# Performance work log

Measured on AMD Instinct MI355X. Metric: run time of the kernel, lower is better.

Reference implementation:

```python
import jax, jax.numpy as jnp
import numpy as np

D_MODEL = 768
NUM_HEADS = 12
D_HEAD = D_MODEL // NUM_HEADS


def setup_inputs() -> dict:
    key = jax.random.key(0)
    ks = jax.random.split(key, 12)
    B, S = 2, 2048
    s = 1.0 / np.sqrt(D_MODEL)
    inp = {
        "query": jax.random.normal(ks[0], (B, S, D_MODEL), dtype=jnp.float32),
        "key": jax.random.normal(ks[1], (B, S, D_MODEL), dtype=jnp.float32),
        "value": jax.random.normal(ks[2], (B, S, D_MODEL), dtype=jnp.float32),
        "mask": jax.random.randint(ks[3], (B, 1, 1, S), 0, 2, dtype=jnp.int32),
        "Wq": jax.random.normal(ks[4], (D_MODEL, D_MODEL), dtype=jnp.float32) * s,
        "bq": jnp.zeros((D_MODEL,), dtype=jnp.float32),
        "Wk": jax.random.normal(ks[5], (D_MODEL, D_MODEL), dtype=jnp.float32) * s,
        "bk": jnp.zeros((D_MODEL,), dtype=jnp.float32),
        "Wv": jax.random.normal(ks[6], (D_MODEL, D_MODEL), dtype=jnp.float32) * s,
        "bv": jnp.zeros((D_MODEL,), dtype=jnp.float32),
        "Wo": jax.random.normal(ks[7], (D_MODEL, D_MODEL), dtype=jnp.float32) * s,
        "bo": jnp.zeros((D_MODEL,), dtype=jnp.float32),
    }
    return inp


def _split_heads(x):
    # [B, S, D] -> [B, H, S, Dh]
    B, S, _ = x.shape
    return x.reshape(B, S, NUM_HEADS, D_HEAD).transpose(0, 2, 1, 3)


def reference(query, key, value, mask, Wq, bq, Wk, bk, Wv, bv, Wo, bo):
    q = _split_heads(query @ Wq + bq)
    k = _split_heads(key @ Wk + bk)
    v = _split_heads(value @ Wv + bv)
    scores = jnp.einsum("bhqd,bhkd->bhqk", q, k) / jnp.sqrt(jnp.float32(D_HEAD))
    scores = jnp.where(mask == 0, -jnp.inf, scores)
    attn = jax.nn.softmax(scores, axis=-1)  # dropout is identity at inference
    ctx = jnp.einsum("bhqk,bhkd->bhqd", attn, v)
    B, _, S, _ = ctx.shape
    ctx = ctx.transpose(0, 2, 1, 3).reshape(B, S, D_MODEL)
    return ctx @ Wo + bo
```

## Files before the change

kernel.cpp:

```cpp
#include <hip/hip_runtime.h>
#include <stdint.h>

#define D_MODEL 768
#define SEQ     2048
#define BATCH   2
#define NHEAD   12
#define DHEAD   64
#define MROWS   (BATCH * SEQ)

typedef __bf16 bf16x8 __attribute__((ext_vector_type(8)));
typedef float  f32x4  __attribute__((ext_vector_type(4)));
typedef unsigned short u16;
typedef u16 u16x4 __attribute__((ext_vector_type(4)));
typedef uint32_t u32;

__device__ __forceinline__ u16 f32_to_bf16(float x) {
    u32 u = __float_as_uint(x);
    u32 r = (u + 0x7FFFu + ((u >> 16) & 1u)) >> 16;
    return (u16)r;
}
__device__ __forceinline__ float bf16_to_f32(u16 h) {
    return __uint_as_float(((u32)h) << 16);
}
__device__ __forceinline__ void split2(float x, u16 &hi, u16 &lo) {
    hi = f32_to_bf16(x);
    lo = f32_to_bf16(x - bf16_to_f32(hi));
}
__device__ __forceinline__ u32 pack2(float a, float b) {
    return ((u32)f32_to_bf16(b) << 16) | (u32)f32_to_bf16(a);
}

__device__ __forceinline__ void stage16(const u16* g, const u16* l) {
    __builtin_amdgcn_global_load_lds(
        (const __attribute__((address_space(1))) u32*)g,
        (__attribute__((address_space(3))) u32*)l,
        16, 0, 0);
}

#define QSCALE 0.1803368801111204f
#define MSHIFT 20.0f

__global__ void prep_split_x(const float* __restrict__ q, const float* __restrict__ k,
                             const float* __restrict__ v, u16* __restrict__ xbase)
{
    const int t = blockIdx.y;
    const float* src = (t == 0) ? q : (t == 1) ? k : v;
    const size_t P = (size_t)MROWS * D_MODEL;
    u16* xh = xbase + (size_t)t * 2 * P;
    u16* xl = xh + P;
    size_t idx = ((size_t)blockIdx.x * 256 + threadIdx.x) * 4;
    float4 val = *reinterpret_cast<const float4*>(&src[idx]);
    float vv[4] = {val.x, val.y, val.z, val.w};
    u16x4 h4, l4;
    #pragma unroll
    for (int j = 0; j < 4; ++j) { u16 h, l; split2(vv[j], h, l); h4[j] = h; l4[j] = l; }
    *reinterpret_cast<u16x4*>(&xh[idx]) = h4;
    *reinterpret_cast<u16x4*>(&xl[idx]) = l4;
}

__global__ void prep_wt(const float* __restrict__ Wq, const float* __restrict__ Wk,
                        const float* __restrict__ Wv, const float* __restrict__ Wo,
                        u16* __restrict__ wtbase)
{
    const int w = blockIdx.z;
    const float* W = (w == 0) ? Wq : (w == 1) ? Wk : (w == 2) ? Wv : Wo;
    const size_t WP = (size_t)D_MODEL * D_MODEL;
    u16* th = wtbase + (size_t)w * 2 * WP;
    u16* tl = th + WP;

    __shared__ float tile[32][33];
    const int tx = threadIdx.x & 31, ty = threadIdx.x >> 5;
    const int n0 = blockIdx.x * 32, k0 = blockIdx.y * 32;
    #pragma unroll
    for (int r = 0; r < 4; ++r) {
        int kk = k0 + ty + r * 8;
        tile[ty + r * 8][tx] = W[(size_t)kk * D_MODEL + n0 + tx];
    }
    __syncthreads();
    #pragma unroll
    for (int r = 0; r < 4; ++r) {
        int n = n0 + ty + r * 8;
        float v = tile[tx][ty + r * 8];
        u16 h, l; split2(v, h, l);
        th[(size_t)n * D_MODEL + k0 + tx] = h;
        tl[(size_t)n * D_MODEL + k0 + tx] = l;
    }
}

__global__ void prep_bias(const int* __restrict__ Mask, float* __restrict__ BiasM)
{
    int i = blockIdx.x * 256 + threadIdx.x;
    BiasM[i] = (Mask[i] == 0) ? -3e38f : -MSHIFT;
}

__global__ __launch_bounds__(256, 4) void gemm3(
    const u16* __restrict__ Ah0, const u16* __restrict__ Al0,
    const u16* __restrict__ Ah1, const u16* __restrict__ Al1,
    const u16* __restrict__ Ah2, const u16* __restrict__ Al2,
    const u16* __restrict__ Bh0, const u16* __restrict__ Bl0,
    const u16* __restrict__ Bh1, const u16* __restrict__ Bl1,
    const u16* __restrict__ Bh2, const u16* __restrict__ Bl2,
    const float* __restrict__ bias0, const float* __restrict__ bias1,
    const float* __restrict__ bias2,
    u16* __restrict__ Qhl, u16* __restrict__ Khl, u16* __restrict__ Vt,
    float* __restrict__ Out, int mode)
{
    const int z = (mode == 3) ? 3 : (int)blockIdx.z;
    const u16 *GAh, *GAl, *GBh, *GBl; const float* Bias;
    if (z == 1)      { GAh = Ah1; GAl = Al1; GBh = Bh1; GBl = Bl1; Bias = bias1; }
    else if (z == 2) { GAh = Ah2; GAl = Al2; GBh = Bh2; GBl = Bl2; Bias = bias2; }
    else             { GAh = Ah0; GAl = Al0; GBh = Bh0; GBl = Bl0; Bias = bias0; }

    const int m0 = blockIdx.y * 128;
    const int n0 = blockIdx.x * 64;
    const int tid  = threadIdx.x;
    const int wave = tid >> 6, lane = tid & 63;
    const int quad = lane >> 4, l16 = lane & 15;
    const int wm = wave & 1, wn = wave >> 1;

    __shared__ u16 sAh[128 * 32];
    __shared__ u16 sAl[128 * 32];
    __shared__ u16 sBh[64 * 32];
    __shared__ u16 sBl[64 * 32];

    const int srow = lane >> 2;
    const int sc8  = (lane & 3) * 8;

    f32x4 acc[4][2] = {};

    for (int k0 = 0; k0 < D_MODEL; k0 += 32) {
        {
            #pragma unroll
            for (int i = 0; i < 2; ++i) {
                int row = wave * 32 + i * 16 + srow;
                size_t ga = (size_t)(m0 + row) * D_MODEL + k0 + sc8;
                int ldst = (wave * 32 + i * 16) * 32;
                stage16(&GAh[ga], &sAh[ldst]);
                stage16(&GAl[ga], &sAl[ldst]);
            }
            int row = wave * 16 + srow;
            size_t gb = (size_t)(n0 + row) * D_MODEL + k0 + sc8;
            int ldst = (wave * 16) * 32;
            stage16(&GBh[gb], &sBh[ldst]);
            stage16(&GBl[gb], &sBl[ldst]);
        }
        asm volatile("s_waitcnt vmcnt(0)" ::: "memory");
        __syncthreads();

        bf16x8 afh[4], afl[4], bfh[2], bfl[2];
        #pragma unroll
        for (int t = 0; t < 4; ++t) {
            int ar = wm * 64 + t * 16 + l16;
            afh[t] = *reinterpret_cast<const bf16x8*>(&sAh[ar * 32 + quad * 8]);
            afl[t] = *reinterpret_cast<const bf16x8*>(&sAl[ar * 32 + quad * 8]);
        }
        #pragma unroll
        for (int t = 0; t < 2; ++t) {
            int bc = wn * 32 + t * 16 + l16;
            bfh[t] = *reinterpret_cast<const bf16x8*>(&sBh[bc * 32 + quad * 8]);
            bfl[t] = *reinterpret_cast<const bf16x8*>(&sBl[bc * 32 + quad * 8]);
        }
        #pragma unroll
        for (int mt = 0; mt < 4; ++mt) {
            #pragma unroll
            for (int nt = 0; nt < 2; ++nt) {
                f32x4 a = acc[mt][nt];
                a = __builtin_amdgcn_mfma_f32_16x16x32_bf16(afh[mt], bfh[nt], a, 0, 0, 0);
                a = __builtin_amdgcn_mfma_f32_16x16x32_bf16(afh[mt], bfl[nt], a, 0, 0, 0);
                a = __builtin_amdgcn_mfma_f32_16x16x32_bf16(afl[mt], bfh[nt], a, 0, 0, 0);
                acc[mt][nt] = a;
            }
        }
        __syncthreads();
    }

    #pragma unroll
    for (int nt = 0; nt < 2; ++nt) {
        int n = n0 + wn * 32 + nt * 16 + l16;
        float bv = Bias[n];
        #pragma unroll
        for (int mt = 0; mt < 4; ++mt) {
            #pragma unroll
            for (int r = 0; r < 4; ++r) {
                int m = m0 + wm * 64 + mt * 16 + quad * 4 + r;
                float v = acc[mt][nt][r] + bv;
                if (mode == 3) {
                    Out[(size_t)m * D_MODEL + n] = v;
                } else {
                    int b = m >> 11, s = m & (SEQ - 1);
                    int h = n >> 6, d = n & 63;
                    size_t bh = (size_t)(b * NHEAD + h);
                    if (z == 0) {
                        u16 hi, lo; split2(v * QSCALE, hi, lo);
                        u16* base = &Qhl[(bh * SEQ + s) * 128];
                        base[d] = hi; base[d + 64] = lo;
                    } else if (z == 1) {
                        u16 hi, lo; split2(v, hi, lo);
                        u16* base = &Khl[(bh * SEQ + s) * 128];
                        base[d] = hi; base[d + 64] = lo;
                    } else {
                        Vt[(bh * DHEAD + d) * SEQ + s] = f32_to_bf16(v);
                    }
                }
            }
        }
    }
}

__global__ __launch_bounds__(256, 6) void attn_kernel(
    const u16* __restrict__ Qhl, const u16* __restrict__ Khl, const u16* __restrict__ Vt,
    const float* __restrict__ BiasM, float* __restrict__ Opart,
    float* __restrict__ Lpart)
{
    const int qt   = blockIdx.x;
    const int bh   = blockIdx.y;
    const int half = blockIdx.z;
    const int b    = bh / NHEAD;
    const int tid  = threadIdx.x;
    const int wave = tid >> 6, lane = tid & 63;
    const int quad = lane >> 4, l16 = lane & 15;

    __shared__ u16 sK[4 * 2048];
    __shared__ u16 sV[2 * 2048];

    const u16* qbase = &Qhl[((size_t)bh * SEQ + qt * 64 + wave * 16 + l16) * 128];
    bf16x8 qh0 = *reinterpret_cast<const bf16x8*>(&qbase[quad * 8]);
    bf16x8 qh1 = *reinterpret_cast<const bf16x8*>(&qbase[32 + quad * 8]);
    bf16x8 ql0 = *reinterpret_cast<const bf16x8*>(&qbase[64 + quad * 8]);
    bf16x8 ql1 = *reinterpret_cast<const bf16x8*>(&qbase[96 + quad * 8]);

    float lrow = 0.f;
    f32x4 oacc[4] = {};

    const float* biasb = &BiasM[b * SEQ];
    const int srcl0 = (((quad * 2) & 3) << 4) | l16;
    const int srcl1 = (((quad * 2 + 1) & 3) << 4) | l16;
    const bool selhi = (quad >> 1) != 0;

    const int strow = wave * 16 + (lane >> 2);
    const int stc8  = (lane & 3) * 8;
    const u16* kgb = &Khl[(size_t)bh * SEQ * 128];
    const u16* vgb = &Vt[(size_t)bh * DHEAD * SEQ];

    const int kvbeg = half * (SEQ / 2);
    for (int kv0 = kvbeg; kv0 < kvbeg + SEQ / 2; kv0 += 64) {
        #pragma unroll
        for (int j = 0; j < 4; ++j)
            stage16(&kgb[(size_t)(kv0 + strow) * 128 + j * 32 + stc8],
                    &sK[j * 2048 + wave * 512]);
        #pragma unroll
        for (int j = 0; j < 2; ++j)
            stage16(&vgb[(size_t)strow * SEQ + kv0 + j * 32 + stc8],
                    &sV[j * 2048 + wave * 512]);
        asm volatile("s_waitcnt vmcnt(0)" ::: "memory");
        __syncthreads();

        f32x4 sacc[4];
        #pragma unroll
        for (int mt = 0; mt < 4; ++mt) {
            float4 b4 = *reinterpret_cast<const float4*>(
                &biasb[kv0 + mt * 16 + quad * 4]);
            sacc[mt][0] = b4.x; sacc[mt][1] = b4.y;
            sacc[mt][2] = b4.z; sacc[mt][3] = b4.w;
        }
        #pragma unroll
        for (int mt = 0; mt < 4; ++mt) {
            const int rb = (mt * 16 + l16) * 32 + quad * 8;
            bf16x8 kh0 = *reinterpret_cast<const bf16x8*>(&sK[rb]);
            bf16x8 kh1 = *reinterpret_cast<const bf16x8*>(&sK[2048 + rb]);
            bf16x8 kl0 = *reinterpret_cast<const bf16x8*>(&sK[4096 + rb]);
            bf16x8 kl1 = *reinterpret_cast<const bf16x8*>(&sK[6144 + rb]);
            f32x4 s = sacc[mt];
            s = __builtin_amdgcn_mfma_f32_16x16x32_bf16(kh0, qh0, s, 0, 0, 0);
            s = __builtin_amdgcn_mfma_f32_16x16x32_bf16(kh1, qh1, s, 0, 0, 0);
            s = __builtin_amdgcn_mfma_f32_16x16x32_bf16(kh0, ql0, s, 0, 0, 0);
            s = __builtin_amdgcn_mfma_f32_16x16x32_bf16(kh1, ql1, s, 0, 0, 0);
            s = __builtin_amdgcn_mfma_f32_16x16x32_bf16(kl0, qh0, s, 0, 0, 0);
            s = __builtin_amdgcn_mfma_f32_16x16x32_bf16(kl1, qh1, s, 0, 0, 0);
            sacc[mt] = s;
        }

        u32 pLo[4], pHi[4];
        #pragma unroll
        for (int mt = 0; mt < 4; ++mt) {
            float p0 = exp2f(sacc[mt][0]);
            float p1 = exp2f(sacc[mt][1]);
            float p2 = exp2f(sacc[mt][2]);
            float p3 = exp2f(sacc[mt][3]);
            lrow += (p0 + p1) + (p2 + p3);
            pLo[mt] = pack2(p0, p1);
            pHi[mt] = pack2(p2, p3);
        }

        union FU { u32 u[4]; bf16x8 v; } fr[2];
        #pragma unroll
        for (int f = 0; f < 2; ++f) {
            u32 a, bb;
            a  = (u32)__shfl((int)pLo[2 * f],     srcl0, 64);
            bb = (u32)__shfl((int)pLo[2 * f + 1], srcl0, 64);
            fr[f].u[0] = selhi ? bb : a;
            a  = (u32)__shfl((int)pHi[2 * f],     srcl0, 64);
            bb = (u32)__shfl((int)pHi[2 * f + 1], srcl0, 64);
            fr[f].u[1] = selhi ? bb : a;
            a  = (u32)__shfl((int)pLo[2 * f],     srcl1, 64);
            bb = (u32)__shfl((int)pLo[2 * f + 1], srcl1, 64);
            fr[f].u[2] = selhi ? bb : a;
            a  = (u32)__shfl((int)pHi[2 * f],     srcl1, 64);
            bb = (u32)__shfl((int)pHi[2 * f + 1], srcl1, 64);
            fr[f].u[3] = selhi ? bb : a;
        }

        #pragma unroll
        for (int dt = 0; dt < 4; ++dt) {
            const int rb = (dt * 16 + l16) * 32 + quad * 8;
            bf16x8 vb0 = *reinterpret_cast<const bf16x8*>(&sV[rb]);
            bf16x8 vb1 = *reinterpret_cast<const bf16x8*>(&sV[2048 + rb]);
            oacc[dt] = __builtin_amdgcn_mfma_f32_16x16x32_bf16(vb0, fr[0].v, oacc[dt], 0, 0, 0);
            oacc[dt] = __builtin_amdgcn_mfma_f32_16x16x32_bf16(vb1, fr[1].v, oacc[dt], 0, 0, 0);
        }
        __syncthreads();
    }

    lrow += __shfl_xor(lrow, 16, 64);
    lrow += __shfl_xor(lrow, 32, 64);

    size_t rowb = ((size_t)(half * (BATCH * NHEAD) + bh)) * SEQ
                + qt * 64 + wave * 16 + l16;
    float* ob = &Opart[rowb * 64];
    #pragma unroll
    for (int dt = 0; dt < 4; ++dt)
        *reinterpret_cast<f32x4*>(&ob[dt * 16 + quad * 4]) = oacc[dt];
    if (quad == 0) Lpart[rowb] = lrow;
}

__global__ void attn_combine(const float* __restrict__ Opart,
                             const float* __restrict__ Lpart,
                             u16* __restrict__ CTXh, u16* __restrict__ CTXl)
{
    const int NROW = BATCH * NHEAD * SEQ;
    int t = blockIdx.x * 256 + threadIdx.x;
    int row = t >> 4;
    int d0 = (t & 15) << 2;
    float inv = 1.f / (Lpart[row] + Lpart[NROW + row]);
    f32x4 O0 = *reinterpret_cast<const f32x4*>(&Opart[(size_t)row * 64 + d0]);
    f32x4 O1 = *reinterpret_cast<const f32x4*>(&Opart[((size_t)NROW + row) * 64 + d0]);
    int bh = row >> 11, q = row & (SEQ - 1);
    int b = bh / NHEAD, h = bh % NHEAD;
    size_t off = ((size_t)(b * SEQ + q)) * D_MODEL + h * DHEAD + d0;
    u16x4 h4, l4;
    #pragma unroll
    for (int j = 0; j < 4; ++j) {
        float val = (O0[j] + O1[j]) * inv;
        u16 hi, lo; split2(val, hi, lo);
        h4[j] = hi; l4[j] = lo;
    }
    *reinterpret_cast<u16x4*>(&CTXh[off]) = h4;
    *reinterpret_cast<u16x4*>(&CTXl[off]) = l4;
}

extern "C" void kernel_launch(void* const* d_in, const int* in_sizes, int n_in,
                              void* d_out, int out_size, void* d_ws, size_t ws_size,
                              hipStream_t stream)
{
    const float* query = (const float*)d_in[0];
    const float* key   = (const float*)d_in[1];
    const float* value = (const float*)d_in[2];
    const int*   mask  = (const int*)d_in[3];
    const float* Wq = (const float*)d_in[4];
    const float* bq = (const float*)d_in[5];
    const float* Wk = (const float*)d_in[6];
    const float* bk = (const float*)d_in[7];
    const float* Wv = (const float*)d_in[8];
    const float* bv = (const float*)d_in[9];
    const float* Wo = (const float*)d_in[10];
    const float* bo = (const float*)d_in[11];

    char* ws = (char*)d_ws;
    const size_t P2  = (size_t)MROWS * D_MODEL * 2;
    const size_t WP2 = (size_t)D_MODEL * D_MODEL * 2;

    u16* Xbase = (u16*)ws;
    u16* Xh_q = Xbase;                       u16* Xl_q = (u16*)((char*)Xh_q + P2);
    u16* Xh_k = (u16*)((char*)Xbase + 2*P2); u16* Xl_k = (u16*)((char*)Xh_k + P2);
    u16* Xh_v = (u16*)((char*)Xbase + 4*P2); u16* Xl_v = (u16*)((char*)Xh_v + P2);

    char* wtb = ws + 6 * P2;
    u16* Wh_q = (u16*)wtb;                   u16* Wl_q = (u16*)(wtb + WP2);
    u16* Wh_k = (u16*)(wtb + 2*WP2);         u16* Wl_k = (u16*)(wtb + 3*WP2);
    u16* Wh_v = (u16*)(wtb + 4*WP2);         u16* Wl_v = (u16*)(wtb + 5*WP2);
    u16* Wh_o = (u16*)(wtb + 6*WP2);         u16* Wl_o = (u16*)(wtb + 7*WP2);

    char* qb = wtb + 8 * WP2;
    const size_t QK_BYTES = (size_t)BATCH * NHEAD * SEQ * 128 * 2;
    u16* QhlBuf = (u16*)qb;
    u16* KhlBuf = (u16*)(qb + QK_BYTES);
    u16* VtBuf  = (u16*)(qb + 2 * QK_BYTES);

    char* tail = qb + 2 * QK_BYTES + QK_BYTES / 2;
    float* BiasM = (float*)tail;
    float* Lpart = (float*)(tail + 16384);

    float* Opart = (float*)Xh_k;
    u16* CTXh = Xh_q; u16* CTXl = Xl_q;

    float* out = (float*)d_out;
    dim3 blk(256, 1, 1);

    prep_split_x<<<dim3(3072, 3), blk, 0, stream>>>(query, key, value, Xbase);
    prep_wt<<<dim3(24, 24, 4), blk, 0, stream>>>(Wq, Wk, Wv, Wo, (u16*)wtb);
    prep_bias<<<dim3(16), blk, 0, stream>>>(mask, BiasM);

    gemm3<<<dim3(12, 32, 3), blk, 0, stream>>>(
        Xh_q, Xl_q, Xh_k, Xl_k, Xh_v, Xl_v,
        Wh_q, Wl_q, Wh_k, Wl_k, Wh_v, Wl_v,
        bq, bk, bv, QhlBuf, KhlBuf, VtBuf, nullptr, 0);

    attn_kernel<<<dim3(32, 24, 2), blk, 0, stream>>>(
        QhlBuf, KhlBuf, VtBuf, BiasM, Opart, Lpart);

    attn_combine<<<dim3(3072), blk, 0, stream>>>(Opart, Lpart, CTXh, CTXl);

    gemm3<<<dim3(12, 32, 1), blk, 0, stream>>>(
        CTXh, CTXl, nullptr, nullptr, nullptr, nullptr,
        Wh_o, Wl_o, nullptr, nullptr, nullptr, nullptr,
        bo, nullptr, nullptr, nullptr, nullptr, nullptr, out, 3);
}
```

Baseline: 310.8 us.

## Process two query groups per wave in attention and swap GEMM grid order

The attention kernel now gives each wave 32 query rows (two 16-row groups) instead of 16, so each staged K/V tile in shared memory is reused twice. This halves the number of blocks and the global-to-LDS traffic per query. The cost is doubled accumulator registers, so occupancy is lowered to 3 blocks per CU. Separately, the GEMM grid is transposed so consecutive blocks walk along M rather than N, which changes L2 reuse of the weight tiles.

```diff
diff --git a/kernel.cpp b/kernel.cpp
--- a/kernel.cpp
+++ b/kernel.cpp
@@ -111,8 +111,8 @@
     else if (z == 2) { GAh = Ah2; GAl = Al2; GBh = Bh2; GBl = Bl2; Bias = bias2; }
     else             { GAh = Ah0; GAl = Al0; GBh = Bh0; GBl = Bl0; Bias = bias0; }
 
-    const int m0 = blockIdx.y * 128;
-    const int n0 = blockIdx.x * 64;
+    const int m0 = blockIdx.x * 128;
+    const int n0 = blockIdx.y * 64;
     const int tid  = threadIdx.x;
     const int wave = tid >> 6, lane = tid & 63;
     const int quad = lane >> 4, l16 = lane & 15;
@@ -207,7 +207,7 @@
     }
 }
 
-__global__ __launch_bounds__(256, 6) void attn_kernel(
+__global__ __launch_bounds__(256, 3) void attn_kernel(
     const u16* __restrict__ Qhl, const u16* __restrict__ Khl, const u16* __restrict__ Vt,
     const float* __restrict__ BiasM, float* __restrict__ Opart,
     float* __restrict__ Lpart)
@@ -223,14 +223,18 @@
     __shared__ u16 sK[4 * 2048];
     __shared__ u16 sV[2 * 2048];
 
-    const u16* qbase = &Qhl[((size_t)bh * SEQ + qt * 64 + wave * 16 + l16) * 128];
-    bf16x8 qh0 = *reinterpret_cast<const bf16x8*>(&qbase[quad * 8]);
-    bf16x8 qh1 = *reinterpret_cast<const bf16x8*>(&qbase[32 + quad * 8]);
-    bf16x8 ql0 = *reinterpret_cast<const bf16x8*>(&qbase[64 + quad * 8]);
-    bf16x8 ql1 = *reinterpret_cast<const bf16x8*>(&qbase[96 + quad * 8]);
-
-    float lrow = 0.f;
-    f32x4 oacc[4] = {};
+    bf16x8 qh0[2], qh1[2], ql0[2], ql1[2];
+    #pragma unroll
+    for (int g = 0; g < 2; ++g) {
+        const u16* qbase = &Qhl[((size_t)bh * SEQ + qt * 128 + wave * 32 + g * 16 + l16) * 128];
+        qh0[g] = *reinterpret_cast<const bf16x8*>(&qbase[quad * 8]);
+        qh1[g] = *reinterpret_cast<const bf16x8*>(&qbase[32 + quad * 8]);
+        ql0[g] = *reinterpret_cast<const bf16x8*>(&qbase[64 + quad * 8]);
+        ql1[g] = *reinterpret_cast<const bf16x8*>(&qbase[96 + quad * 8]);
+    }
+
+    float lrow[2] = {0.f, 0.f};
+    f32x4 oacc[2][4] = {};
 
     const float* biasb = &BiasM[b * SEQ];
     const int srcl0 = (((quad * 2) & 3) << 4) | l16;
@@ -255,82 +259,90 @@
         asm volatile("s_waitcnt vmcnt(0)" ::: "memory");
         __syncthreads();
 
-        f32x4 sacc[4];
+        f32x4 binit[4];
         #pragma unroll
         for (int mt = 0; mt < 4; ++mt) {
             float4 b4 = *reinterpret_cast<const float4*>(
                 &biasb[kv0 + mt * 16 + quad * 4]);
-            sacc[mt][0] = b4.x; sacc[mt][1] = b4.y;
-            sacc[mt][2] = b4.z; sacc[mt][3] = b4.w;
-        }
-        #pragma unroll
-        for (int mt = 0; mt < 4; ++mt) {
-            const int rb = (mt * 16 + l16) * 32 + quad * 8;
-            bf16x8 kh0 = *reinterpret_cast<const bf16x8*>(&sK[rb]);
-            bf16x8 kh1 = *reinterpret_cast<const bf16x8*>(&sK[2048 + rb]);
-            bf16x8 kl0 = *reinterpret_cast<const bf16x8*>(&sK[4096 + rb]);
-            bf16x8 kl1 = *reinterpret_cast<const bf16x8*>(&sK[6144 + rb]);
-            f32x4 s = sacc[mt];
-            s = __builtin_amdgcn_mfma_f32_16x16x32_bf16(kh0, qh0, s, 0, 0, 0);
-            s = __builtin_amdgcn_mfma_f32_16x16x32_bf16(kh1, qh1, s, 0, 0, 0);
-            s = __builtin_amdgcn_mfma_f32_16x16x32_bf16(kh0, ql0, s, 0, 0, 0);
-            s = __builtin_amdgcn_mfma_f32_16x16x32_bf16(kh1, ql1, s, 0, 0, 0);
-            s = __builtin_amdgcn_mfma_f32_16x16x32_bf16(kl0, qh0, s, 0, 0, 0);
-            s = __builtin_amdgcn_mfma_f32_16x16x32_bf16(kl1, qh1, s, 0, 0, 0);
-            sacc[mt] = s;
-        }
-
-        u32 pLo[4], pHi[4];
-        #pragma unroll
-        for (int mt = 0; mt < 4; ++mt) {
-            float p0 = exp2f(sacc[mt][0]);
-            float p1 = exp2f(sacc[mt][1]);
-            float p2 = exp2f(sacc[mt][2]);
-            float p3 = exp2f(sacc[mt][3]);
-            lrow += (p0 + p1) + (p2 + p3);
-            pLo[mt] = pack2(p0, p1);
-            pHi[mt] = pack2(p2, p3);
-        }
-
-        union FU { u32 u[4]; bf16x8 v; } fr[2];
-        #pragma unroll
-        for (int f = 0; f < 2; ++f) {
-            u32 a, bb;
-            a  = (u32)__shfl((int)pLo[2 * f],     srcl0, 64);
-            bb = (u32)__shfl((int)pLo[2 * f + 1], srcl0, 64);
-            fr[f].u[0] = selhi ? bb : a;
-            a  = (u32)__shfl((int)pHi[2 * f],     srcl0, 64);
-            bb = (u32)__shfl((int)pHi[2 * f + 1], srcl0, 64);
-            fr[f].u[1] = selhi ? bb : a;
-            a  = (u32)__shfl((int)pLo[2 * f],     srcl1, 64);
-            bb = (u32)__shfl((int)pLo[2 * f + 1], srcl1, 64);
-            fr[f].u[2] = selhi ? bb : a;
-            a  = (u32)__shfl((int)pHi[2 * f],     srcl1, 64);
-            bb = (u32)__shfl((int)pHi[2 * f + 1], srcl1, 64);
-            fr[f].u[3] = selhi ? bb : a;
-        }
-
-        #pragma unroll
-        for (int dt = 0; dt < 4; ++dt) {
-            const int rb = (dt * 16 + l16) * 32 + quad * 8;
-            bf16x8 vb0 = *reinterpret_cast<const bf16x8*>(&sV[rb]);
-            bf16x8 vb1 = *reinterpret_cast<const bf16x8*>(&sV[2048 + rb]);
-            oacc[dt] = __builtin_amdgcn_mfma_f32_16x16x32_bf16(vb0, fr[0].v, oacc[dt], 0, 0, 0);
-            oacc[dt] = __builtin_amdgcn_mfma_f32_16x16x32_bf16(vb1, fr[1].v, oacc[dt], 0, 0, 0);
+            binit[mt][0] = b4.x; binit[mt][1] = b4.y;
+            binit[mt][2] = b4.z; binit[mt][3] = b4.w;
+        }
+
+        #pragma unroll
+        for (int g = 0; g < 2; ++g) {
+            f32x4 sacc[4];
+            #pragma unroll
+            for (int mt = 0; mt < 4; ++mt) {
+                const int rb = (mt * 16 + l16) * 32 + quad * 8;
+                bf16x8 kh0 = *reinterpret_cast<const bf16x8*>(&sK[rb]);
+                bf16x8 kh1 = *reinterpret_cast<const bf16x8*>(&sK[2048 + rb]);
+                bf16x8 kl0 = *reinterpret_cast<const bf16x8*>(&sK[4096 + rb]);
+                bf16x8 kl1 = *reinterpret_cast<const bf16x8*>(&sK[6144 + rb]);
+                f32x4 s = binit[mt];
+                s = __builtin_amdgcn_mfma_f32_16x16x32_bf16(kh0, qh0[g], s, 0, 0, 0);
+                s = __builtin_amdgcn_mfma_f32_16x16x32_bf16(kh1, qh1[g], s, 0, 0, 0);
+                s = __builtin_amdgcn_mfma_f32_16x16x32_bf16(kh0, ql0[g], s, 0, 0, 0);
+                s = __builtin_amdgcn_mfma_f32_16x16x32_bf16(kh1, ql1[g], s, 0, 0, 0);
+                s = __builtin_amdgcn_mfma_f32_16x16x32_bf16(kl0, qh0[g], s, 0, 0, 0);
+                s = __builtin_amdgcn_mfma_f32_16x16x32_bf16(kl1, qh1[g], s, 0, 0, 0);
+                sacc[mt] = s;
+            }
+
+            u32 pLo[4], pHi[4];
+            #pragma unroll
+            for (int mt = 0; mt < 4; ++mt) {
+                float p0 = exp2f(sacc[mt][0]);
+                float p1 = exp2f(sacc[mt][1]);
+                float p2 = exp2f(sacc[mt][2]);
+                float p3 = exp2f(sacc[mt][3]);
+                lrow[g] += (p0 + p1) + (p2 + p3);
+                pLo[mt] = pack2(p0, p1);
+                pHi[mt] = pack2(p2, p3);
+            }
+
+            union FU { u32 u[4]; bf16x8 v; } fr[2];
+            #pragma unroll
+            for (int f = 0; f < 2; ++f) {
+                u32 a, bb;
+                a  = (u32)__shfl((int)pLo[2 * f],     srcl0, 64);
+                bb = (u32)__shfl((int)pLo[2 * f + 1], srcl0, 64);
+                fr[f].u[0] = selhi ? bb : a;
+                a  = (u32)__shfl((int)pHi[2 * f],     srcl0, 64);
+                bb = (u32)__shfl((int)pHi[2 * f + 1], srcl0, 64);
+                fr[f].u[1] = selhi ? bb : a;
+                a  = (u32)__shfl((int)pLo[2 * f],     srcl1, 64);
+                bb = (u32)__shfl((int)pLo[2 * f + 1], srcl1, 64);
+                fr[f].u[2] = selhi ? bb : a;
+                a  = (u32)__shfl((int)pHi[2 * f],     srcl1, 64);
+                bb = (u32)__shfl((int)pHi[2 * f + 1], srcl1, 64);
+                fr[f].u[3] = selhi ? bb : a;
+            }
+
+            #pragma unroll
+            for (int dt = 0; dt < 4; ++dt) {
+                const int rb = (dt * 16 + l16) * 32 + quad * 8;
+                bf16x8 vb0 = *reinterpret_cast<const bf16x8*>(&sV[rb]);
+                bf16x8 vb1 = *reinterpret_cast<const bf16x8*>(&sV[2048 + rb]);
+                oacc[g][dt] = __builtin_amdgcn_mfma_f32_16x16x32_bf16(vb0, fr[0].v, oacc[g][dt], 0, 0, 0);
+                oacc[g][dt] = __builtin_amdgcn_mfma_f32_16x16x32_bf16(vb1, fr[1].v, oacc[g][dt], 0, 0, 0);
+            }
         }
         __syncthreads();
     }
 
-    lrow += __shfl_xor(lrow, 16, 64);
-    lrow += __shfl_xor(lrow, 32, 64);
-
-    size_t rowb = ((size_t)(half * (BATCH * NHEAD) + bh)) * SEQ
-                + qt * 64 + wave * 16 + l16;
-    float* ob = &Opart[rowb * 64];
-    #pragma unroll
-    for (int dt = 0; dt < 4; ++dt)
-        *reinterpret_cast<f32x4*>(&ob[dt * 16 + quad * 4]) = oacc[dt];
-    if (quad == 0) Lpart[rowb] = lrow;
+    #pragma unroll
+    for (int g = 0; g < 2; ++g) {
+        float l = lrow[g];
+        l += __shfl_xor(l, 16, 64);
+        l += __shfl_xor(l, 32, 64);
+        size_t rowb = ((size_t)(half * (BATCH * NHEAD) + bh)) * SEQ
+                    + qt * 128 + wave * 32 + g * 16 + l16;
+        float* ob = &Opart[rowb * 64];
+        #pragma unroll
+        for (int dt = 0; dt < 4; ++dt)
+            *reinterpret_cast<f32x4*>(&ob[dt * 16 + quad * 4]) = oacc[g][dt];
+        if (quad == 0) Lpart[rowb] = l;
+    }
 }
 
 __global__ void attn_combine(const float* __restrict__ Opart,
@@ -410,17 +422,17 @@
     prep_wt<<<dim3(24, 24, 4), blk, 0, stream>>>(Wq, Wk, Wv, Wo, (u16*)wtb);
     prep_bias<<<dim3(16), blk, 0, stream>>>(mask, BiasM);
 
-    gemm3<<<dim3(12, 32, 3), blk, 0, stream>>>(
+    gemm3<<<dim3(32, 12, 3), blk, 0, stream>>>(
         Xh_q, Xl_q, Xh_k, Xl_k, Xh_v, Xl_v,
         Wh_q, Wl_q, Wh_k, Wl_k, Wh_v, Wl_v,
         bq, bk, bv, QhlBuf, KhlBuf, VtBuf, nullptr, 0);
 
-    attn_kernel<<<dim3(32, 24, 2), blk, 0, stream>>>(
+    attn_kernel<<<dim3(16, 24, 2), blk, 0, stream>>>(
         QhlBuf, KhlBuf, VtBuf, BiasM, Opart, Lpart);
 
     attn_combine<<<dim3(3072), blk, 0, stream>>>(Opart, Lpart, CTXh, CTXl);
 
-    gemm3<<<dim3(12, 32, 1), blk, 0, stream>>>(
+    gemm3<<<dim3(32, 12, 1), blk, 0, stream>>>(
         CTXh, CTXl, nullptr, nullptr, nullptr, nullptr,
         Wh_o, Wl_o, nullptr, nullptr, nullptr, nullptr,
         bo, nullptr, nullptr, nullptr, nullptr, nullptr, out, 3);
```

Measured after the change: 281.9 us. 1.1x faster.
